# Performance work log

Hardware: AMD Instinct MI355X
Metric: run time of the kernel (lower is better)

The kernel has to match this reference:

```python
import jax, jax.numpy as jnp
import numpy as np

B, L, C = 2, 4096, 1024
H, WIN = 16, 128            # num_heads, window_size (each side)
D = C // H                  # head_dim = 64


def setup_inputs() -> dict:
    key = jax.random.key(0)
    ks = jax.random.split(key, 9)
    s = 0.02
    return {
        "x": jax.random.normal(ks[0], (B, L, C), jnp.float32),
        # Linear weights stored as [in, out] (y = x @ W + b), same math as torch Linear.
        "wq": jax.random.normal(ks[1], (C, C), jnp.float32) * s,
        "bq": jnp.zeros((C,), jnp.float32),
        "wk": jax.random.normal(ks[2], (C, C), jnp.float32) * s,
        "bk": jnp.zeros((C,), jnp.float32),
        "wv": jax.random.normal(ks[3], (C, C), jnp.float32) * s,
        "bv": jnp.zeros((C,), jnp.float32),
        "wo": jax.random.normal(ks[4], (C, C), jnp.float32) * s,
        "bo": jnp.zeros((C,), jnp.float32),
    }


def reference(x, wq, bq, wk, bk, wv, bv, wo, bo):
    b, l, c = x.shape
    nb = l // WIN

    def heads(t):  # (B,L,C) -> (B,H,L,D)
        return t.reshape(b, l, H, D).transpose(0, 2, 1, 3)

    q = heads(x @ wq + bq)
    k = heads(x @ wk + bk)
    v = heads(x @ wv + bv)

    # and ARE included in the softmax, exactly as the original module does).
    kp = jnp.pad(k, ((0, 0), (0, 0), (WIN, WIN), (0, 0)))
    vp = jnp.pad(v, ((0, 0), (0, 0), (WIN, WIN), (0, 0)))

    idx = np.arange(nb)[:, None] * WIN + np.arange(3 * WIN)[None, :]  # [nb, 3W]
    kb = kp[:, :, idx]  # [B,H,nb,3W,D]
    vb = vp[:, :, idx]  # [B,H,nb,3W,D]
    qb = q.reshape(b, H, nb, WIN, D)

    scores = jnp.einsum('bhnqd,bhnkd->bhnqk', qb, kb) / float(np.sqrt(D))
    r = np.arange(WIN)[:, None]
    col = np.arange(3 * WIN)[None, :]
    band = jnp.asarray(np.abs(col - r - WIN) <= WIN)
    scores = jnp.where(band, scores, -jnp.inf)
    probs = jax.nn.softmax(scores, axis=-1)

    out = jnp.einsum('bhnqk,bhnkd->bhnqd', probs, vb)
    out = out.reshape(b, H, l, D).transpose(0, 2, 1, 3).reshape(b, l, c)
    return out @ wo + bo
```

## Files before the change

### kernel.cpp

```cpp
#include <hip/hip_runtime.h>

using short8  = __attribute__((ext_vector_type(8))) short;
using short4v = __attribute__((ext_vector_type(4))) short;
using floatx4 = __attribute__((ext_vector_type(4))) float;

#define MFMA_B16(a, b, c) __builtin_amdgcn_mfma_f32_16x16x32_bf16(a, b, c, 0, 0, 0)

__device__ __forceinline__ short f2bf(float f) {
  union { float f; unsigned u; } v; v.f = f;
  unsigned r = v.u + 0x7fffu + ((v.u >> 16) & 1u);
  return (short)(r >> 16);
}
__device__ __forceinline__ short f2bf_rtz(float f) {
  union { float f; unsigned u; } v; v.f = f;
  return (short)(v.u >> 16);
}

__device__ __forceinline__ void gload_lds16(const short* g, short* l) {
  __builtin_amdgcn_global_load_lds(
      (const __attribute__((address_space(1))) unsigned int*)g,
      (__attribute__((address_space(3))) unsigned int*)l, 16, 0, 0);
}

__global__ __launch_bounds__(256) void prep(
    const float4* __restrict__ x, short4v* __restrict__ xb,
    const float* __restrict__ w0, const float* __restrict__ w1,
    const float* __restrict__ w2, const float* __restrict__ w3,
    short* __restrict__ wT) {
  __shared__ float tile[32][33];
  int blk = blockIdx.x;
  if (blk < 8192) {
    int i = blk * 256 + threadIdx.x;
    float4 v = x[i];
    short4v o = { f2bf(v.x), f2bf(v.y), f2bf(v.z), f2bf(v.w) };
    xb[i] = o;
  } else {
    int r = blk - 8192;
    int z = r >> 10; r &= 1023;
    const float* w = z == 0 ? w0 : (z == 1 ? w1 : (z == 2 ? w2 : w3));
    short* out = wT + (size_t)z * 1024 * 1024;
    int n0 = (r & 31) * 32, k0 = (r >> 5) * 32;
    int tx = threadIdx.x & 31, ty = threadIdx.x >> 5;
#pragma unroll
    for (int i = 0; i < 4; ++i)
      tile[ty + i * 8][tx] = w[(size_t)(k0 + ty + i * 8) * 1024 + n0 + tx];
    __syncthreads();
#pragma unroll
    for (int i = 0; i < 4; ++i)
      out[(size_t)(n0 + ty + i * 8) * 1024 + k0 + tx] = f2bf(tile[tx][ty + i * 8]);
  }
}

__device__ __forceinline__ void gemm_core_256x256(
    const short* __restrict__ Ag0, const short* __restrict__ Bg0,
    short* As , short* Bs ,
    floatx4 (&acc)[8][4]) {
  const int tid = threadIdx.x;
  const int w = tid >> 6, lane = tid & 63, quad = lane >> 4, l16 = lane & 15;
  const int wm = w >> 2, wn = w & 3;
  const int srow = tid >> 3;
  const int scol = ((tid & 7) ^ (srow & 7)) * 8;

  floatx4 zf = {0.f, 0.f, 0.f, 0.f};
#pragma unroll
  for (int i = 0; i < 8; ++i)
#pragma unroll
    for (int j = 0; j < 4; ++j) acc[i][j] = zf;

  const short* gA = Ag0 + (size_t)srow * 1024 + scol;
  const short* gB = Bg0 + (size_t)srow * 1024 + scol;

  auto stA = [&](int buf, int q, int kt) {
    gload_lds16(gA + (size_t)q * 64 * 1024 + kt * 64,
                As + buf * 16384 + q * 4096 + w * 512);
  };
  auto stB = [&](int buf, int q, int kt) {
    gload_lds16(gB + (size_t)q * 64 * 1024 + kt * 64,
                Bs + buf * 16384 + q * 4096 + w * 512);
  };

  short8 aF[8], bF[8];
  auto ldA = [&](int buf, int mh) {
    const char* base = (const char*)(As + buf * 16384);
#pragma unroll
    for (int m = 0; m < 4; ++m)
#pragma unroll
      for (int kk = 0; kk < 2; ++kk) {
        int row = wm * 128 + mh * 64 + m * 16 + l16;
        int off = row * 128 + kk * 64 + quad * 16;
        off ^= (row & 7) << 4;
        aF[m * 2 + kk] = *(const short8*)(base + off);
      }
  };
  auto ldB = [&](int buf, int nh) {
    const char* base = (const char*)(Bs + buf * 16384);
#pragma unroll
    for (int n = 0; n < 2; ++n)
#pragma unroll
      for (int kk = 0; kk < 2; ++kk) {
        int row = wn * 64 + nh * 32 + n * 16 + l16;
        int off = row * 128 + kk * 64 + quad * 16;
        off ^= (row & 7) << 4;
        bF[(nh * 2 + n) * 2 + kk] = *(const short8*)(base + off);
      }
  };
  auto mm = [&](int mh, int nh) {
#pragma unroll
    for (int m = 0; m < 4; ++m)
#pragma unroll
      for (int n = 0; n < 2; ++n)
#pragma unroll
        for (int kk = 0; kk < 2; ++kk)
          acc[mh * 4 + m][nh * 2 + n] =
              MFMA_B16(aF[m * 2 + kk], bF[(nh * 2 + n) * 2 + kk],
                       acc[mh * 4 + m][nh * 2 + n]);
  };

  stA(0, 0, 0); stA(0, 1, 0); stA(0, 2, 0); stA(0, 3, 0);
  stB(0, 0, 0); stB(0, 1, 0); stB(0, 2, 0); stB(0, 3, 0);
  stA(1, 0, 1); stA(1, 1, 1); stA(1, 2, 1); stA(1, 3, 1);
  stB(1, 0, 1); stB(1, 1, 1); stB(1, 2, 1); stB(1, 3, 1);
  asm volatile("s_waitcnt vmcnt(8)" ::: "memory");
  __builtin_amdgcn_s_barrier();

#pragma unroll 2
  for (int t = 0; t < 16; ++t) {
    const int cb = t & 1;
    ldA(cb, 0);
    ldB(cb, 0);
    __builtin_amdgcn_s_barrier();
    __builtin_amdgcn_s_setprio(1);
    mm(0, 0);
    __builtin_amdgcn_s_setprio(0);
    __builtin_amdgcn_s_barrier();
    ldB(cb, 1);
    if (t + 2 < 16) { stA(cb, 0, t + 2); stA(cb, 2, t + 2); }
    __builtin_amdgcn_s_barrier();
    __builtin_amdgcn_s_setprio(1);
    mm(0, 1);
    __builtin_amdgcn_s_setprio(0);
    __builtin_amdgcn_s_barrier();
    ldA(cb, 1);
    if (t + 2 < 16) {
      stB(cb, 0, t + 2); stB(cb, 1, t + 2);
      stB(cb, 2, t + 2); stB(cb, 3, t + 2);
    }
    __builtin_amdgcn_s_barrier();
    __builtin_amdgcn_s_setprio(1);
    mm(1, 0);
    __builtin_amdgcn_s_setprio(0);
    __builtin_amdgcn_s_barrier();
    if (t + 2 < 16) {
      stA(cb, 1, t + 2); stA(cb, 3, t + 2);
      __builtin_amdgcn_s_setprio(1);
      mm(1, 1);
      __builtin_amdgcn_s_setprio(0);
      asm volatile("s_waitcnt vmcnt(8)" ::: "memory");
    } else {
      __builtin_amdgcn_s_setprio(1);
      mm(1, 1);
      __builtin_amdgcn_s_setprio(0);
      asm volatile("s_waitcnt vmcnt(0)" ::: "memory");
    }
    __builtin_amdgcn_s_barrier();
  }
}

__global__ __launch_bounds__(512, 2) void gemm_qkv(
    const short* __restrict__ xb, const short* __restrict__ wT,
    const float* __restrict__ bq, const float* __restrict__ bk,
    const float* __restrict__ bv, short* __restrict__ qkv) {
  __shared__ __align__(16) short As[2 * 16384];
  __shared__ __align__(16) short Bs[2 * 16384];
  int bid = blockIdx.x;
  int xcd = bid & 7;
  int idx = bid >> 3;
  int z   = idx >> 4;
  int r   = idx & 15;
  int mb  = xcd * 4 + (r & 3);
  int nb  = r >> 2;
  const short* wt = wT + (size_t)z * 1024 * 1024;
  const float* bias = z == 0 ? bq : (z == 1 ? bk : bv);
  short* out = qkv + (size_t)z * 8192 * 1024;
  int m0 = mb * 256, n0 = nb * 256;

  floatx4 acc[8][4];
  gemm_core_256x256(xb + (size_t)m0 * 1024, wt + (size_t)n0 * 1024, As, Bs, acc);

  int tid = threadIdx.x, w = tid >> 6, lane = tid & 63, quad = lane >> 4, l16 = lane & 15;
  int wm = w >> 2, wn = w & 3;
  float qs = (z == 0) ? 0.125f * 1.44269504f : 1.0f;
#pragma unroll
  for (int mf = 0; mf < 8; ++mf)
#pragma unroll
    for (int nf = 0; nf < 4; ++nf)
#pragma unroll
      for (int rg = 0; rg < 4; ++rg) {
        int m = m0 + wm * 128 + mf * 16 + quad * 4 + rg;
        int cc = n0 + wn * 64 + nf * 16 + l16;
        float v = (acc[mf][nf][rg] + bias[cc]) * qs;
        int b = m >> 12, l = m & 4095;
        int hh = cc >> 6, d = cc & 63;
        out[((size_t)(b * 16 + hh) * 4096 + l) * 64 + d] = f2bf(v);
      }
}

__global__ __launch_bounds__(256) void attn_kern(const short* __restrict__ qkv,
                                                 short* __restrict__ attnb) {
  const int L = 4096, H = 16;
  int n = blockIdx.x, h = blockIdx.y, b = blockIdx.z;
  const size_t hs = (size_t)L * 64;
  const short* Qp = qkv + (size_t)(b * H + h) * hs;
  const short* Kp = qkv + (size_t)8192 * 1024 + (size_t)(b * H + h) * hs;
  const short* Vp = qkv + (size_t)2 * 8192 * 1024 + (size_t)(b * H + h) * hs;

  __shared__ __align__(16) short kt[128][72];
  __shared__ __align__(16) short vt[64][136];
  __shared__ __align__(16) short pl[4][32][136];

  int tid = threadIdx.x, w = tid >> 6, lane = tid & 63, quad = lane >> 4, l16 = lane & 15;

  short8 onesf;
  {
    short ov = (l16 == 0) ? (short)0x3F80 : (short)0;
#pragma unroll
    for (int j = 0; j < 8; ++j) onesf[j] = ov;
  }

  short8 qf[2][2];
#pragma unroll
  for (int rt = 0; rt < 2; ++rt)
#pragma unroll
    for (int ks = 0; ks < 2; ++ks)
      qf[rt][ks] = *(const short8*)(Qp + (size_t)(n * 128 + w * 32 + rt * 16 + l16) * 64 + ks * 32 + quad * 8);

  floatx4 zf = {0.f, 0.f, 0.f, 0.f};
  floatx4 o[2][4];
  floatx4 osum[2];
#pragma unroll
  for (int i = 0; i < 2; ++i) {
    osum[i] = zf;
#pragma unroll
    for (int j = 0; j < 4; ++j) o[i][j] = zf;
  }

#pragma unroll
  for (int c = 0; c < 3; ++c) {
    int bk = n - 1 + c;
    bool inr = (c == 1) || (c == 0 ? (n > 0) : (n < 31));
    __syncthreads();
    if (inr) {
      const short* kc_ = Kp + (size_t)bk * 128 * 64;
      int kr = tid >> 2, ksg = (tid & 3) * 16;
#pragma unroll
      for (int p = 0; p < 2; ++p) {
        int r2 = p * 64 + kr;
        *(short8*)(&kt[r2][ksg])     = *(const short8*)(kc_ + r2 * 64 + ksg);
        *(short8*)(&kt[r2][ksg + 8]) = *(const short8*)(kc_ + r2 * 64 + ksg + 8);
      }
      const short* vc_ = Vp + (size_t)bk * 128 * 64;
      int vkey = tid & 31, vsg = (tid >> 5) * 8;
#pragma unroll
      for (int p = 0; p < 4; ++p) {
        int r2 = p * 32 + vkey;
        short8 vv = *(const short8*)(vc_ + r2 * 64 + vsg);
#pragma unroll
        for (int j = 0; j < 8; ++j) vt[vsg + j][r2] = vv[j];
      }
    } else {
      short8 z8 = {0, 0, 0, 0, 0, 0, 0, 0};
      int kr = tid >> 2, ksg = (tid & 3) * 16;
#pragma unroll
      for (int p = 0; p < 2; ++p) {
        int r2 = p * 64 + kr;
        *(short8*)(&kt[r2][ksg])     = z8;
        *(short8*)(&kt[r2][ksg + 8]) = z8;
      }
      int vr = tid >> 2, vsg2 = (tid & 3) * 32;
#pragma unroll
      for (int q2 = 0; q2 < 4; ++q2) *(short8*)(&vt[vr][vsg2 + q2 * 8]) = z8;
    }
    __syncthreads();

    floatx4 s[2][8];
#pragma unroll
    for (int rt = 0; rt < 2; ++rt)
#pragma unroll
      for (int ct = 0; ct < 8; ++ct) s[rt][ct] = zf;
#pragma unroll
    for (int ct = 0; ct < 8; ++ct) {
      bool any = (c == 0) ? (ct >= w * 2) : (c == 2) ? (ct <= w * 2 + 1) : true;
      if (any) {
        short8 kf0 = *(const short8*)(&kt[ct * 16 + l16][quad * 8]);
        short8 kf1 = *(const short8*)(&kt[ct * 16 + l16][32 + quad * 8]);
#pragma unroll
        for (int rt = 0; rt < 2; ++rt) {
          bool valid = (c == 0) ? (ct >= w * 2 + rt) : (c == 2) ? (ct <= w * 2 + rt) : true;
          if (valid) {
            s[rt][ct] = MFMA_B16(qf[rt][0], kf0, s[rt][ct]);
            s[rt][ct] = MFMA_B16(qf[rt][1], kf1, s[rt][ct]);
          }
        }
      }
    }

#pragma unroll
    for (int rt = 0; rt < 2; ++rt) {
      int wrt = w * 2 + rt;
#pragma unroll
      for (int ct = 0; ct < 8; ++ct) {
        bool tileMasked = (c == 0) ? (ct < wrt) : (c == 2) ? (ct > wrt) : false;
        bool ksDead = (c == 0) ? (2 * (ct >> 1) + 1 < wrt)
                    : (c == 2) ? (2 * (ct >> 1) > wrt) : false;
        bool diag = (c != 1) && (ct == wrt);
        if (ksDead) continue;
        if (tileMasked) {
#pragma unroll
          for (int rg = 0; rg < 4; ++rg)
            pl[w][rt * 16 + quad * 4 + rg][ct * 16 + l16] = 0;
        } else if (diag) {
#pragma unroll
          for (int rg = 0; rg < 4; ++rg) {
            int r16 = quad * 4 + rg;
            float p = exp2f(s[rt][ct][rg]);
            if (c == 0) p = (l16 < r16) ? 0.f : p;
            else        p = (l16 > r16) ? 0.f : p;
            pl[w][rt * 16 + r16][ct * 16 + l16] = f2bf_rtz(p);
          }
        } else {
#pragma unroll
          for (int rg = 0; rg < 4; ++rg)
            pl[w][rt * 16 + quad * 4 + rg][ct * 16 + l16] = f2bf_rtz(exp2f(s[rt][ct][rg]));
        }
      }
    }

    __syncthreads();

#pragma unroll
    for (int ks = 0; ks < 4; ++ks) {
      bool anyrt = (c == 0) ? (2 * ks + 1 >= w * 2) : (c == 2) ? (2 * ks <= w * 2 + 1) : true;
      if (!anyrt) continue;
      short8 vf[4];
#pragma unroll
      for (int ct = 0; ct < 4; ++ct)
        vf[ct] = *(const short8*)(&vt[ct * 16 + l16][ks * 32 + quad * 8]);
#pragma unroll
      for (int rt = 0; rt < 2; ++rt) {
        int wrt = w * 2 + rt;
        bool ksDead = (c == 0) ? (2 * ks + 1 < wrt) : (c == 2) ? (2 * ks > wrt) : false;
        if (ksDead) continue;
        short8 pf = *(const short8*)(&pl[w][rt * 16 + l16][ks * 32 + quad * 8]);
#pragma unroll
        for (int ct = 0; ct < 4; ++ct) o[rt][ct] = MFMA_B16(pf, vf[ct], o[rt][ct]);
        osum[rt] = MFMA_B16(pf, onesf, osum[rt]);
      }
    }
  }

#pragma unroll
  for (int rt = 0; rt < 2; ++rt) {
#pragma unroll
    for (int rg = 0; rg < 4; ++rg) {
      float ssum = __shfl(osum[rt][rg], lane & 48);
      float inv = 1.f / ssum;
      int r = n * 128 + w * 32 + rt * 16 + quad * 4 + rg;
#pragma unroll
      for (int ct = 0; ct < 4; ++ct)
        attnb[(size_t)(b * L + r) * 1024 + h * 64 + ct * 16 + l16] =
            f2bf(o[rt][ct][rg] * inv);
    }
  }
}

__global__ __launch_bounds__(512, 2) void gemm_out(
    const short* __restrict__ attnb, const short* __restrict__ wTo,
    const float* __restrict__ bo, float* __restrict__ outp) {
  __shared__ __align__(16) short As[2 * 16384];
  __shared__ __align__(16) short Bs[2 * 16384];
  int bid = blockIdx.x;
  int xcd = bid & 7;
  int idx = bid >> 3;
  int mb  = xcd * 4 + (idx & 3);
  int nb  = idx >> 2;
  int m0 = mb * 256, n0 = nb * 256;

  floatx4 acc[8][4];
  gemm_core_256x256(attnb + (size_t)m0 * 1024, wTo + (size_t)n0 * 1024, As, Bs, acc);

  int tid = threadIdx.x, w = tid >> 6, lane = tid & 63, quad = lane >> 4, l16 = lane & 15;
  int wm = w >> 2, wn = w & 3;
#pragma unroll
  for (int mf = 0; mf < 8; ++mf)
#pragma unroll
    for (int nf = 0; nf < 4; ++nf)
#pragma unroll
      for (int rg = 0; rg < 4; ++rg) {
        int m = m0 + wm * 128 + mf * 16 + quad * 4 + rg;
        int cc = n0 + wn * 64 + nf * 16 + l16;
        outp[(size_t)m * 1024 + cc] = acc[mf][nf][rg] + bo[cc];
      }
}

extern "C" void kernel_launch(void* const* d_in, const int* in_sizes, int n_in,
                              void* d_out, int out_size, void* d_ws, size_t ws_size,
                              hipStream_t stream) {
  const float* x  = (const float*)d_in[0];
  const float* wq = (const float*)d_in[1];
  const float* bq = (const float*)d_in[2];
  const float* wk = (const float*)d_in[3];
  const float* bk = (const float*)d_in[4];
  const float* wv = (const float*)d_in[5];
  const float* bv = (const float*)d_in[6];
  const float* wo = (const float*)d_in[7];
  const float* bo = (const float*)d_in[8];

  char* ws = (char*)d_ws;
  short* xb    = (short*)ws;
  short* wT    = (short*)(ws + (16u << 20));
  short* qkv   = (short*)(ws + (24u << 20));
  short* attnb = (short*)(ws + (72u << 20));

  prep<<<12288, 256, 0, stream>>>((const float4*)x, (short4v*)xb, wq, wk, wv, wo, wT);
  gemm_qkv<<<384, 512, 0, stream>>>(xb, wT, bq, bk, bv, qkv);
  attn_kern<<<dim3(32, 16, 2), 256, 0, stream>>>(qkv, attnb);
  gemm_out<<<128, 512, 0, stream>>>(attnb, wT + 3u * 1024 * 1024, bo, (float*)d_out);
}
```

Measured before the change: 231.5 us.

## Fuse Q/K/V tiles sharing A loads and shrink out-projection tile for more blocks

The QKV GEMM now computes a 256x128 tile for all three projections in one block, loading each A tile once and reusing it across Q, K and V weight tiles. The grid drops from 384 to 256 blocks, which removes the redundant x reads and leaves fewer partial waves. The output GEMM moves from 256x256 to 128x256 tiles so it launches 256 blocks instead of 128 and fills more CUs. It also gets its own pipeline with B prefetched one step ahead. The costs are higher register pressure from 96 accumulators in the QKV kernel, more LDS for three B buffers, and less reuse per block in the output GEMM.

```diff
diff --git a/kernel.cpp b/kernel.cpp
--- a/kernel.cpp
+++ b/kernel.cpp
@@ -51,10 +51,20 @@
   }
 }
 
-__device__ __forceinline__ void gemm_core_256x256(
-    const short* __restrict__ Ag0, const short* __restrict__ Bg0,
-    short* As , short* Bs ,
-    floatx4 (&acc)[8][4]) {
+__global__ __launch_bounds__(512, 2) void gemm_qkv(
+    const short* __restrict__ xb, const short* __restrict__ wT,
+    const float* __restrict__ bq, const float* __restrict__ bk,
+    const float* __restrict__ bv, short* __restrict__ qkv) {
+  __shared__ __align__(16) short As[2 * 16384];
+  __shared__ __align__(16) short Bs[2 * 3 * 8192];
+
+  int bid = blockIdx.x;
+  int xcd = bid & 7;
+  int idx = bid >> 3;
+  int mb  = xcd * 4 + (idx & 3);
+  int nb  = idx >> 2;
+  int m0 = mb * 256, n0 = nb * 128;
+
   const int tid = threadIdx.x;
   const int w = tid >> 6, lane = tid & 63, quad = lane >> 4, l16 = lane & 15;
   const int wm = w >> 2, wn = w & 3;
@@ -62,24 +72,25 @@
   const int scol = ((tid & 7) ^ (srow & 7)) * 8;
 
   floatx4 zf = {0.f, 0.f, 0.f, 0.f};
-#pragma unroll
-  for (int i = 0; i < 8; ++i)
-#pragma unroll
-    for (int j = 0; j < 4; ++j) acc[i][j] = zf;
-
-  const short* gA = Ag0 + (size_t)srow * 1024 + scol;
-  const short* gB = Bg0 + (size_t)srow * 1024 + scol;
+  floatx4 acc[3][8][2];
+#pragma unroll
+  for (int z = 0; z < 3; ++z)
+#pragma unroll
+    for (int i = 0; i < 8; ++i) { acc[z][i][0] = zf; acc[z][i][1] = zf; }
+
+  const short* gA = xb + (size_t)(m0 + srow) * 1024 + scol;
+  const short* gB0 = wT + (size_t)(n0 + srow) * 1024 + scol;
 
   auto stA = [&](int buf, int q, int kt) {
     gload_lds16(gA + (size_t)q * 64 * 1024 + kt * 64,
                 As + buf * 16384 + q * 4096 + w * 512);
   };
-  auto stB = [&](int buf, int q, int kt) {
-    gload_lds16(gB + (size_t)q * 64 * 1024 + kt * 64,
-                Bs + buf * 16384 + q * 4096 + w * 512);
-  };
-
-  short8 aF[8], bF[8];
+  auto stB = [&](int buf, int z, int q, int kt) {
+    gload_lds16(gB0 + (size_t)z * 1024 * 1024 + (size_t)q * 64 * 1024 + kt * 64,
+                Bs + (buf * 3 + z) * 8192 + q * 4096 + w * 512);
+  };
+
+  short8 aF[8], bF[4];
   auto ldA = [&](int buf, int mh) {
     const char* base = (const char*)(As + buf * 16384);
 #pragma unroll
@@ -92,117 +103,94 @@
         aF[m * 2 + kk] = *(const short8*)(base + off);
       }
   };
-  auto ldB = [&](int buf, int nh) {
-    const char* base = (const char*)(Bs + buf * 16384);
+  auto ldB = [&](int buf, int z) {
+    const char* base = (const char*)(Bs + (buf * 3 + z) * 8192);
 #pragma unroll
     for (int n = 0; n < 2; ++n)
 #pragma unroll
       for (int kk = 0; kk < 2; ++kk) {
-        int row = wn * 64 + nh * 32 + n * 16 + l16;
+        int row = wn * 32 + n * 16 + l16;
         int off = row * 128 + kk * 64 + quad * 16;
         off ^= (row & 7) << 4;
-        bF[(nh * 2 + n) * 2 + kk] = *(const short8*)(base + off);
-      }
-  };
-  auto mm = [&](int mh, int nh) {
+        bF[n * 2 + kk] = *(const short8*)(base + off);
+      }
+  };
+  auto mm = [&](int z, int mh) {
 #pragma unroll
     for (int m = 0; m < 4; ++m)
 #pragma unroll
       for (int n = 0; n < 2; ++n)
 #pragma unroll
         for (int kk = 0; kk < 2; ++kk)
-          acc[mh * 4 + m][nh * 2 + n] =
-              MFMA_B16(aF[m * 2 + kk], bF[(nh * 2 + n) * 2 + kk],
-                       acc[mh * 4 + m][nh * 2 + n]);
+          acc[z][mh * 4 + m][n] =
+              MFMA_B16(aF[m * 2 + kk], bF[n * 2 + kk], acc[z][mh * 4 + m][n]);
   };
 
   stA(0, 0, 0); stA(0, 1, 0); stA(0, 2, 0); stA(0, 3, 0);
-  stB(0, 0, 0); stB(0, 1, 0); stB(0, 2, 0); stB(0, 3, 0);
-  stA(1, 0, 1); stA(1, 1, 1); stA(1, 2, 1); stA(1, 3, 1);
-  stB(1, 0, 1); stB(1, 1, 1); stB(1, 2, 1); stB(1, 3, 1);
+  stB(0, 0, 0, 0); stB(0, 0, 1, 0); stB(0, 1, 0, 0); stB(0, 1, 1, 0);
+  stB(0, 2, 0, 0); stB(0, 2, 1, 0);
+  stA(1, 0, 1); stA(1, 2, 1); stA(1, 1, 1); stA(1, 3, 1);
+  stB(1, 0, 0, 1); stB(1, 0, 1, 1); stB(1, 1, 0, 1); stB(1, 1, 1, 1);
   asm volatile("s_waitcnt vmcnt(8)" ::: "memory");
   __builtin_amdgcn_s_barrier();
 
 #pragma unroll 2
   for (int t = 0; t < 16; ++t) {
-    const int cb = t & 1;
+    const int cb = t & 1, nbuf = cb ^ 1;
     ldA(cb, 0);
     ldB(cb, 0);
-    __builtin_amdgcn_s_barrier();
-    __builtin_amdgcn_s_setprio(1);
-    mm(0, 0);
-    __builtin_amdgcn_s_setprio(0);
+    if (t + 1 < 16) { stB(nbuf, 2, 0, t + 1); stB(nbuf, 2, 1, t + 1); }
+    __builtin_amdgcn_s_setprio(1); mm(0, 0); __builtin_amdgcn_s_setprio(0);
     __builtin_amdgcn_s_barrier();
     ldB(cb, 1);
     if (t + 2 < 16) { stA(cb, 0, t + 2); stA(cb, 2, t + 2); }
-    __builtin_amdgcn_s_barrier();
-    __builtin_amdgcn_s_setprio(1);
-    mm(0, 1);
-    __builtin_amdgcn_s_setprio(0);
+    __builtin_amdgcn_s_setprio(1); mm(1, 0); __builtin_amdgcn_s_setprio(0);
+    __builtin_amdgcn_s_barrier();
+    ldB(cb, 2);
+    __builtin_amdgcn_s_setprio(1); mm(2, 0); __builtin_amdgcn_s_setprio(0);
     __builtin_amdgcn_s_barrier();
     ldA(cb, 1);
-    if (t + 2 < 16) {
-      stB(cb, 0, t + 2); stB(cb, 1, t + 2);
-      stB(cb, 2, t + 2); stB(cb, 3, t + 2);
-    }
-    __builtin_amdgcn_s_barrier();
-    __builtin_amdgcn_s_setprio(1);
-    mm(1, 0);
-    __builtin_amdgcn_s_setprio(0);
-    __builtin_amdgcn_s_barrier();
+    ldB(cb, 0);
+    __builtin_amdgcn_s_setprio(1); mm(0, 1); __builtin_amdgcn_s_setprio(0);
+    __builtin_amdgcn_s_barrier();
+    ldB(cb, 1);
     if (t + 2 < 16) {
       stA(cb, 1, t + 2); stA(cb, 3, t + 2);
-      __builtin_amdgcn_s_setprio(1);
-      mm(1, 1);
-      __builtin_amdgcn_s_setprio(0);
+      stB(cb, 0, 0, t + 2); stB(cb, 0, 1, t + 2);
+    }
+    __builtin_amdgcn_s_setprio(1); mm(1, 1); __builtin_amdgcn_s_setprio(0);
+    __builtin_amdgcn_s_barrier();
+    ldB(cb, 2);
+    if (t + 2 < 16) { stB(cb, 1, 0, t + 2); stB(cb, 1, 1, t + 2); }
+    __builtin_amdgcn_s_setprio(1); mm(2, 1); __builtin_amdgcn_s_setprio(0);
+    if (t + 2 < 16) {
       asm volatile("s_waitcnt vmcnt(8)" ::: "memory");
     } else {
-      __builtin_amdgcn_s_setprio(1);
-      mm(1, 1);
-      __builtin_amdgcn_s_setprio(0);
       asm volatile("s_waitcnt vmcnt(0)" ::: "memory");
     }
     __builtin_amdgcn_s_barrier();
   }
-}
-
-__global__ __launch_bounds__(512, 2) void gemm_qkv(
-    const short* __restrict__ xb, const short* __restrict__ wT,
-    const float* __restrict__ bq, const float* __restrict__ bk,
-    const float* __restrict__ bv, short* __restrict__ qkv) {
-  __shared__ __align__(16) short As[2 * 16384];
-  __shared__ __align__(16) short Bs[2 * 16384];
-  int bid = blockIdx.x;
-  int xcd = bid & 7;
-  int idx = bid >> 3;
-  int z   = idx >> 4;
-  int r   = idx & 15;
-  int mb  = xcd * 4 + (r & 3);
-  int nb  = r >> 2;
-  const short* wt = wT + (size_t)z * 1024 * 1024;
-  const float* bias = z == 0 ? bq : (z == 1 ? bk : bv);
-  short* out = qkv + (size_t)z * 8192 * 1024;
-  int m0 = mb * 256, n0 = nb * 256;
-
-  floatx4 acc[8][4];
-  gemm_core_256x256(xb + (size_t)m0 * 1024, wt + (size_t)n0 * 1024, As, Bs, acc);
-
-  int tid = threadIdx.x, w = tid >> 6, lane = tid & 63, quad = lane >> 4, l16 = lane & 15;
-  int wm = w >> 2, wn = w & 3;
-  float qs = (z == 0) ? 0.125f * 1.44269504f : 1.0f;
-#pragma unroll
-  for (int mf = 0; mf < 8; ++mf)
-#pragma unroll
-    for (int nf = 0; nf < 4; ++nf)
-#pragma unroll
-      for (int rg = 0; rg < 4; ++rg) {
-        int m = m0 + wm * 128 + mf * 16 + quad * 4 + rg;
-        int cc = n0 + wn * 64 + nf * 16 + l16;
-        float v = (acc[mf][nf][rg] + bias[cc]) * qs;
-        int b = m >> 12, l = m & 4095;
-        int hh = cc >> 6, d = cc & 63;
-        out[((size_t)(b * 16 + hh) * 4096 + l) * 64 + d] = f2bf(v);
-      }
+
+  const float* biases[3] = {bq, bk, bv};
+#pragma unroll
+  for (int z = 0; z < 3; ++z) {
+    const float* bias = biases[z];
+    short* out = qkv + (size_t)z * 8192 * 1024;
+    float qs = (z == 0) ? 0.125f * 1.44269504f : 1.0f;
+#pragma unroll
+    for (int mf = 0; mf < 8; ++mf)
+#pragma unroll
+      for (int nf = 0; nf < 2; ++nf)
+#pragma unroll
+        for (int rg = 0; rg < 4; ++rg) {
+          int m = m0 + wm * 128 + mf * 16 + quad * 4 + rg;
+          int cc = n0 + wn * 32 + nf * 16 + l16;
+          float v = (acc[z][mf][nf][rg] + bias[cc]) * qs;
+          int b = m >> 12, l = m & 4095;
+          int hh = cc >> 6, d = cc & 63;
+          out[((size_t)(b * 16 + hh) * 4096 + l) * 64 + d] = f2bf(v);
+        }
+  }
 }
 
 __global__ __launch_bounds__(256) void attn_kern(const short* __restrict__ qkv,
@@ -376,27 +364,112 @@
 __global__ __launch_bounds__(512, 2) void gemm_out(
     const short* __restrict__ attnb, const short* __restrict__ wTo,
     const float* __restrict__ bo, float* __restrict__ outp) {
-  __shared__ __align__(16) short As[2 * 16384];
+  __shared__ __align__(16) short As[2 * 8192];
   __shared__ __align__(16) short Bs[2 * 16384];
+
   int bid = blockIdx.x;
   int xcd = bid & 7;
   int idx = bid >> 3;
-  int mb  = xcd * 4 + (idx & 3);
-  int nb  = idx >> 2;
-  int m0 = mb * 256, n0 = nb * 256;
-
-  floatx4 acc[8][4];
-  gemm_core_256x256(attnb + (size_t)m0 * 1024, wTo + (size_t)n0 * 1024, As, Bs, acc);
-
-  int tid = threadIdx.x, w = tid >> 6, lane = tid & 63, quad = lane >> 4, l16 = lane & 15;
-  int wm = w >> 2, wn = w & 3;
-#pragma unroll
-  for (int mf = 0; mf < 8; ++mf)
+  int mb  = xcd * 8 + (idx & 7);
+  int nb  = idx >> 3;
+  int m0 = mb * 128, n0 = nb * 256;
+
+  const int tid = threadIdx.x;
+  const int w = tid >> 6, lane = tid & 63, quad = lane >> 4, l16 = lane & 15;
+  const int wm = w >> 2, wn = w & 3;
+  const int srow = tid >> 3;
+  const int scol = ((tid & 7) ^ (srow & 7)) * 8;
+
+  floatx4 zf = {0.f, 0.f, 0.f, 0.f};
+  floatx4 acc[4][4];
+#pragma unroll
+  for (int i = 0; i < 4; ++i)
+#pragma unroll
+    for (int j = 0; j < 4; ++j) acc[i][j] = zf;
+
+  const short* gA = attnb + (size_t)(m0 + srow) * 1024 + scol;
+  const short* gB = wTo + (size_t)(n0 + srow) * 1024 + scol;
+
+  auto stA = [&](int buf, int q, int kt) {
+    gload_lds16(gA + (size_t)q * 64 * 1024 + kt * 64,
+                As + buf * 8192 + q * 4096 + w * 512);
+  };
+  auto stB = [&](int buf, int q, int kt) {
+    gload_lds16(gB + (size_t)q * 64 * 1024 + kt * 64,
+                Bs + buf * 16384 + q * 4096 + w * 512);
+  };
+
+  short8 aF[8], bF[4];
+  auto ldA = [&](int buf) {
+    const char* base = (const char*)(As + buf * 8192);
+#pragma unroll
+    for (int m = 0; m < 4; ++m)
+#pragma unroll
+      for (int kk = 0; kk < 2; ++kk) {
+        int row = wm * 64 + m * 16 + l16;
+        int off = row * 128 + kk * 64 + quad * 16;
+        off ^= (row & 7) << 4;
+        aF[m * 2 + kk] = *(const short8*)(base + off);
+      }
+  };
+  auto ldB = [&](int buf, int nh) {
+    const char* base = (const char*)(Bs + buf * 16384);
+#pragma unroll
+    for (int n = 0; n < 2; ++n)
+#pragma unroll
+      for (int kk = 0; kk < 2; ++kk) {
+        int row = wn * 64 + nh * 32 + n * 16 + l16;
+        int off = row * 128 + kk * 64 + quad * 16;
+        off ^= (row & 7) << 4;
+        bF[n * 2 + kk] = *(const short8*)(base + off);
+      }
+  };
+  auto mm = [&](int nh) {
+#pragma unroll
+    for (int m = 0; m < 4; ++m)
+#pragma unroll
+      for (int n = 0; n < 2; ++n)
+#pragma unroll
+        for (int kk = 0; kk < 2; ++kk)
+          acc[m][nh * 2 + n] =
+              MFMA_B16(aF[m * 2 + kk], bF[n * 2 + kk], acc[m][nh * 2 + n]);
+  };
+
+  stA(0, 0, 0); stA(0, 1, 0);
+  stB(0, 0, 0); stB(0, 1, 0); stB(0, 2, 0); stB(0, 3, 0);
+  stA(1, 0, 1); stA(1, 1, 1);
+  asm volatile("s_waitcnt vmcnt(2)" ::: "memory");
+  __builtin_amdgcn_s_barrier();
+
+#pragma unroll 2
+  for (int t = 0; t < 16; ++t) {
+    const int cb = t & 1, nbuf = cb ^ 1;
+    ldA(cb);
+    ldB(cb, 0);
+    if (t + 1 < 16) {
+      stB(nbuf, 0, t + 1); stB(nbuf, 1, t + 1);
+      stB(nbuf, 2, t + 1); stB(nbuf, 3, t + 1);
+    }
+    __builtin_amdgcn_s_setprio(1); mm(0); __builtin_amdgcn_s_setprio(0);
+    __builtin_amdgcn_s_barrier();
+    ldB(cb, 1);
+    if (t + 2 < 16) { stA(cb, 0, t + 2); stA(cb, 1, t + 2); }
+    __builtin_amdgcn_s_setprio(1); mm(1); __builtin_amdgcn_s_setprio(0);
+    if (t + 2 < 16) {
+      asm volatile("s_waitcnt vmcnt(2)" ::: "memory");
+    } else {
+      asm volatile("s_waitcnt vmcnt(0)" ::: "memory");
+    }
+    __builtin_amdgcn_s_barrier();
+  }
+
+#pragma unroll
+  for (int mf = 0; mf < 4; ++mf)
 #pragma unroll
     for (int nf = 0; nf < 4; ++nf)
 #pragma unroll
       for (int rg = 0; rg < 4; ++rg) {
-        int m = m0 + wm * 128 + mf * 16 + quad * 4 + rg;
+        int m = m0 + wm * 64 + mf * 16 + quad * 4 + rg;
         int cc = n0 + wn * 64 + nf * 16 + l16;
         outp[(size_t)m * 1024 + cc] = acc[mf][nf][rg] + bo[cc];
       }
@@ -422,7 +495,7 @@
   short* attnb = (short*)(ws + (72u << 20));
 
   prep<<<12288, 256, 0, stream>>>((const float4*)x, (short4v*)xb, wq, wk, wv, wo, wT);
-  gemm_qkv<<<384, 512, 0, stream>>>(xb, wT, bq, bk, bv, qkv);
+  gemm_qkv<<<256, 512, 0, stream>>>(xb, wT, bq, bk, bv, qkv);
   attn_kern<<<dim3(32, 16, 2), 256, 0, stream>>>(qkv, attnb);
-  gemm_out<<<128, 512, 0, stream>>>(attnb, wT + 3u * 1024 * 1024, bo, (float*)d_out);
-}
+  gemm_out<<<256, 512, 0, stream>>>(attnb, wT + 3u * 1024 * 1024, bo, (float*)d_out);
+}
```

Result: slower. 241.9 us (+4.5%).
